# Optimization experiments

Measured on AMD Instinct MI355X. Metric: run time of the kernel, lower is better.

## Reference

```python
import jax, jax.numpy as jnp
import numpy as np

N_NODES = 50000


def _gcn_layer(x, src, dst, norm_src, norm_dst, W, b, act):
    # DGL GraphConv with norm='both': D_out^{-1/2} A D_in^{-1/2} X W + b
    h = x * norm_src[:, None]                      # scale by src out-degree
    m = h[src]                                     # gather messages [E, d]
    agg = jax.ops.segment_sum(m, dst, num_segments=N_NODES)  # scatter-add
    agg = agg * norm_dst[:, None]
    out = agg @ W + b
    if act:
        out = jax.nn.relu(out)
    return out


def setup_inputs() -> dict:
    key = jax.random.key(0)
    ks = jax.random.split(key, 10)
    E = 800000
    in_size, hid, out_size = 128, 128, 64
    features = jax.random.normal(ks[0], (N_NODES, in_size), dtype=jnp.float32)
    src = jax.random.randint(ks[1], (E,), 0, N_NODES, dtype=jnp.int32)
    dst = jax.random.randint(ks[2], (E,), 0, N_NODES, dtype=jnp.int32)
    s = 0.05
    W1 = jax.random.normal(ks[3], (in_size, hid), dtype=jnp.float32) * s
    b1 = jnp.zeros((hid,), dtype=jnp.float32)
    W2 = jax.random.normal(ks[4], (hid, hid), dtype=jnp.float32) * s
    b2 = jnp.zeros((hid,), dtype=jnp.float32)
    W3 = jax.random.normal(ks[5], (hid, out_size), dtype=jnp.float32) * s
    b3 = jnp.zeros((out_size,), dtype=jnp.float32)
    return {"features": features, "W1": W1, "b1": b1, "W2": W2, "b2": b2,
            "W3": W3, "b3": b3, "src": src, "dst": dst}


def reference(features, W1, b1, W2, b2, W3, b3, src, dst):
    ones = jnp.ones(src.shape, dtype=features.dtype)
    out_deg = jax.ops.segment_sum(ones, src, num_segments=N_NODES)
    in_deg = jax.ops.segment_sum(ones, dst, num_segments=N_NODES)
    norm_src = jnp.maximum(out_deg, 1.0) ** -0.5   # clamp(min=1) as in DGL
    norm_dst = jnp.maximum(in_deg, 1.0) ** -0.5
    h = _gcn_layer(features, src, dst, norm_src, norm_dst, W1, b1, act=True)
    # dropout is identity in eval mode
    h = _gcn_layer(h, src, dst, norm_src, norm_dst, W2, b2, act=True)
    h = _gcn_layer(h, src, dst, norm_src, norm_dst, W3, b3, act=False)
    return h
```

## Files before the change

kernel.cpp:

```cpp
#include <hip/hip_runtime.h>
#include <math.h>

#define N_NODES 50000
#define K_DIM 128
#define CAP 64
#define CHUNK 25000
#define RH 25000
#define HWORDS 12500

typedef __attribute__((ext_vector_type(8))) short short8_t;
typedef __attribute__((ext_vector_type(4))) float f32x4_t;
typedef __attribute__((ext_vector_type(8))) _Float16 half8_t;

__device__ inline unsigned short f2bf(float x) {
    unsigned u = __float_as_uint(x);
    unsigned r = u + 0x7fffu + ((u >> 16) & 1u);
    return (unsigned short)(r >> 16);
}
__device__ inline float bf2f(unsigned short h) {
    return __uint_as_float(((unsigned)h) << 16);
}

__global__ void init_zero_kernel(_Float16* Yx, _Float16* Yy, _Float16* Yz) {
    int t = threadIdx.x;
    if (t < 128) {
        Yx[(size_t)N_NODES * 128 + t] = (_Float16)0.f;
        Yy[(size_t)N_NODES * 128 + t] = (_Float16)0.f;
    }
    if (t < 64) Yz[(size_t)N_NODES * 64 + t] = (_Float16)0.f;
}


__global__ __launch_bounds__(1024) void hist_kernel(const int* __restrict__ src,
                                                    const int* __restrict__ dst, int E,
                                                    unsigned* __restrict__ pin,
                                                    unsigned* __restrict__ pout) {
    __shared__ unsigned h[HWORDS];
    int b  = blockIdx.x >> 2;
    int io = (blockIdx.x >> 1) & 1;
    int r  = blockIdx.x & 1;
    int tid = threadIdx.x;
    for (int t = tid; t < HWORDS; t += 1024) h[t] = 0;
    __syncthreads();
    const int* keys = io ? src : dst;
    int start = b * CHUNK;
    int end = start + CHUNK; if (end > E) end = E;
    int vlo = r * RH;
    for (int i = start + tid; i < end; i += 1024) {
        int v = keys[i] - vlo;
        if ((unsigned)v < (unsigned)RH)
            atomicAdd(&h[v >> 1], 1u << ((v & 1) * 16));
    }
    __syncthreads();
    unsigned* out = io ? pout : pin;
    for (int t = tid; t < HWORDS; t += 1024)
        out[(size_t)b * (2 * HWORDS) + r * HWORDS + t] = h[t];
}

__global__ void offsets_norm_kernel(const unsigned* __restrict__ pin,
                                    const unsigned* __restrict__ pout,
                                    unsigned short* __restrict__ off16,
                                    int* __restrict__ indeg,
                                    float* __restrict__ nsrc, float* __restrict__ ndst,
                                    int n, int NB) {
    int v = blockIdx.x * blockDim.x + threadIdx.x;
    if (v >= n) return;
    int wi = v >> 1, sh = (v & 1) * 16;
    int od = 0;
    for (int b = 0; b < NB; ++b)
        od += (pout[(size_t)b * (2 * HWORDS) + wi] >> sh) & 0xffff;
    int run = 0;
    for (int b = 0; b < NB; ++b) {
        int c = (pin[(size_t)b * (2 * HWORDS) + wi] >> sh) & 0xffff;
        off16[(size_t)b * n + v] = (unsigned short)(run < CAP ? run : CAP);
        run += c;
    }
    indeg[v] = run < CAP ? run : CAP;
    int odc = od < 1 ? 1 : od;
    int idc = run < 1 ? 1 : run;
    nsrc[v] = 1.0f / sqrtf((float)odc);
    ndst[v] = 1.0f / sqrtf((float)idc);
}

__global__ __launch_bounds__(1024) void scatter_kernel(const int* __restrict__ src,
                                                       const int* __restrict__ dst, int E,
                                                       const unsigned short* __restrict__ off16,
                                                       int* __restrict__ csr, int n) {
    __shared__ unsigned cur[HWORDS];
    int b = blockIdx.x >> 1;
    int r = blockIdx.x & 1;
    int tid = threadIdx.x;
    int vlo = r * RH;
    const unsigned short* offb = off16 + (size_t)b * n + vlo;
    for (int t = tid; t < HWORDS; t += 1024)
        cur[t] = (unsigned)offb[2 * t] | ((unsigned)offb[2 * t + 1] << 16);
    __syncthreads();
    int start = b * CHUNK;
    int end = start + CHUNK; if (end > E) end = E;
    for (int i = start + tid; i < end; i += 1024) {
        int v = dst[i];
        int vr = v - vlo;
        if ((unsigned)vr < (unsigned)RH) {
            int sh = (vr & 1) * 16;
            unsigned old = atomicAdd(&cur[vr >> 1], 1u << sh);
            unsigned p = (old >> sh) & 0xffff;
            if (p < CAP) csr[((size_t)v << 6) + p] = src[i];
        }
    }
}

__global__ void split_w_all_kernel(const float* __restrict__ W1,
                                   const float* __restrict__ W2,
                                   const float* __restrict__ W3,
                                   unsigned short* __restrict__ W1h, unsigned short* __restrict__ W1l,
                                   unsigned short* __restrict__ W2h, unsigned short* __restrict__ W2l,
                                   unsigned short* __restrict__ W3h, unsigned short* __restrict__ W3l) {
    int gi = blockIdx.x * blockDim.x + threadIdx.x;
    const float* W; unsigned short *WBh, *WBl; int M, i;
    if (gi < 2048)      { W = W1; WBh = W1h; WBl = W1l; M = 128; i = gi; }
    else if (gi < 4096) { W = W2; WBh = W2h; WBl = W2l; M = 128; i = gi - 2048; }
    else if (gi < 5120) { W = W3; WBh = W3h; WBl = W3l; M = 64;  i = gi - 4096; }
    else return;
    int c    = i >> 8;
    int rem  = i & 255;
    int kc   = rem >> 6;
    int lane = rem & 63;
    int m = lane & 15, q = lane >> 4;
    int n = c * 16 + m;
    #pragma unroll
    for (int j = 0; j < 8; ++j) {
        int k = kc * 32 + q * 8 + j;
        float w = W[(size_t)k * M + n];
        unsigned short hi = f2bf(w);
        unsigned short lo = f2bf(w - bf2f(hi));
        WBh[(size_t)i * 8 + j] = hi;
        WBl[(size_t)i * 8 + j] = lo;
    }
}

template <int M>
__global__ __launch_bounds__(256) void gemm_mfma_kernel(
        const float* __restrict__ X,
        const unsigned short* __restrict__ WBh_,
        const unsigned short* __restrict__ WBl_,
        const float* __restrict__ nsrc, _Float16* __restrict__ Yh, int n) {
    constexpr int LSTR = 136;
    __shared__ short Xhi[64 * LSTR];
    __shared__ short Xlo[64 * LSTR];
    int tid = threadIdx.x;
    int lane = tid & 63, wave = tid >> 6;
    int rowBlock = blockIdx.x * 64;

    #pragma unroll
    for (int l = 0; l < 8; ++l) {
        int idx = (tid + l * 256) * 4;
        int r = idx >> 7;
        int c = idx & 127;
        float4 v = make_float4(0.f, 0.f, 0.f, 0.f);
        int gr = rowBlock + r;
        if (gr < n) v = *(const float4*)&X[(size_t)gr * K_DIM + c];
        unsigned short h0 = f2bf(v.x), h1 = f2bf(v.y), h2 = f2bf(v.z), h3 = f2bf(v.w);
        short4 hs = {(short)h0, (short)h1, (short)h2, (short)h3};
        short4 ls = {(short)f2bf(v.x - bf2f(h0)), (short)f2bf(v.y - bf2f(h1)),
                     (short)f2bf(v.z - bf2f(h2)), (short)f2bf(v.w - bf2f(h3))};
        *(short4*)&Xhi[r * LSTR + c] = hs;
        *(short4*)&Xlo[r * LSTR + c] = ls;
    }
    __syncthreads();

    int m = lane & 15, q = lane >> 4;
    short8_t ah[4], al[4];
    {
        int abase = (wave * 16 + m) * LSTR + q * 8;
        #pragma unroll
        for (int kc = 0; kc < 4; ++kc) {
            ah[kc] = *(const short8_t*)&Xhi[abase + kc * 32];
            al[kc] = *(const short8_t*)&Xlo[abase + kc * 32];
        }
    }
    float ns[4];
    int orow0 = rowBlock + wave * 16 + q * 4;
    #pragma unroll
    for (int r = 0; r < 4; ++r) ns[r] = (orow0 + r < n) ? nsrc[orow0 + r] : 0.f;

    const short8_t* WBh = (const short8_t*)WBh_;
    const short8_t* WBl = (const short8_t*)WBl_;
    constexpr int CT = M / 16;
    #pragma unroll
    for (int c = 0; c < CT; ++c) {
        short8_t bh[4], bl[4];
        #pragma unroll
        for (int kc = 0; kc < 4; ++kc) {
            bh[kc] = WBh[(c * 4 + kc) * 64 + lane];
            bl[kc] = WBl[(c * 4 + kc) * 64 + lane];
        }
        f32x4_t acc = {0.f, 0.f, 0.f, 0.f};
        #pragma unroll
        for (int kc = 0; kc < 4; ++kc) {
            acc = __builtin_amdgcn_mfma_f32_16x16x32_bf16(ah[kc], bh[kc], acc, 0, 0, 0);
            acc = __builtin_amdgcn_mfma_f32_16x16x32_bf16(ah[kc], bl[kc], acc, 0, 0, 0);
            acc = __builtin_amdgcn_mfma_f32_16x16x32_bf16(al[kc], bh[kc], acc, 0, 0, 0);
        }
        int col = c * 16 + m;
        #pragma unroll
        for (int r = 0; r < 4; ++r) {
            int row = orow0 + r;
            if (row < n) Yh[(size_t)row * M + col] = (_Float16)(acc[r] * ns[r]);
        }
    }
}

template <int MOUT>
__global__ __launch_bounds__(256, 3) void agg_gemm_kernel(
        const _Float16* __restrict__ Yin,
        const int* __restrict__ indeg, const int* __restrict__ csr,
        const float* __restrict__ ndst, const float* __restrict__ bias,
        const unsigned short* __restrict__ WBh_,
        const unsigned short* __restrict__ WBl_,
        const float* __restrict__ nsrc, _Float16* __restrict__ Yout, int n) {
    constexpr int LSTR = 136;
    __shared__ short Xhi[32 * LSTR];
    __shared__ short Xlo[32 * LSTR];
    int tid = threadIdx.x;
    int lane = tid & 63, wave = tid >> 6;
    int rowBlock = blockIdx.x * 32;

    int sub = tid >> 4;
    int f8  = (tid & 15) * 8;
    #pragma unroll 1
    for (int p = 0; p < 2; ++p) {
        int r = p * 16 + sub;
        int v = rowBlock + r;
        float o[8] = {};
        if (v < n) {
            int deg = indeg[v];
            const int* __restrict__ row = &csr[(size_t)v * CAP];
            float acc[8] = {};
            #pragma unroll 1
            for (int i = 0; i < deg; i += 16) {
                int idx[16];
                #pragma unroll
                for (int t = 0; t < 16; t += 4) {
                    int4 s4 = *(const int4*)&row[i + t];
                    idx[t + 0] = s4.x; idx[t + 1] = s4.y;
                    idx[t + 2] = s4.z; idx[t + 3] = s4.w;
                }
                #pragma unroll
                for (int t = 1; t < 16; ++t)
                    if (i + t >= deg) idx[t] = N_NODES;
                half8_t g[16];
                #pragma unroll
                for (int t = 0; t < 16; ++t)
                    g[t] = *(const half8_t*)&Yin[(size_t)idx[t] * 128 + f8];
                #pragma unroll
                for (int t = 0; t < 16; ++t) {
                    #pragma unroll
                    for (int j = 0; j < 8; ++j) acc[j] += (float)g[t][j];
                }
            }
            float nd = ndst[v];
            #pragma unroll
            for (int j = 0; j < 8; ++j)
                o[j] = fmaxf(nd * acc[j] + bias[f8 + j], 0.f);
        }
        short hs[8], ls[8];
        #pragma unroll
        for (int j = 0; j < 8; ++j) {
            unsigned short h = f2bf(o[j]);
            hs[j] = (short)h;
            ls[j] = (short)f2bf(o[j] - bf2f(h));
        }
        *(short4*)&Xhi[r * LSTR + f8]     = *(short4*)&hs[0];
        *(short4*)&Xhi[r * LSTR + f8 + 4] = *(short4*)&hs[4];
        *(short4*)&Xlo[r * LSTR + f8]     = *(short4*)&ls[0];
        *(short4*)&Xlo[r * LSTR + f8 + 4] = *(short4*)&ls[4];
    }
    __syncthreads();

    int m = lane & 15, q = lane >> 4;
    int wrow = wave & 1;
    int wcol = wave >> 1;
    short8_t ah[4], al[4];
    {
        int abase = (wrow * 16 + m) * LSTR + q * 8;
        #pragma unroll
        for (int kc = 0; kc < 4; ++kc) {
            ah[kc] = *(const short8_t*)&Xhi[abase + kc * 32];
            al[kc] = *(const short8_t*)&Xlo[abase + kc * 32];
        }
    }
    float ns[4];
    int orow0 = rowBlock + wrow * 16 + q * 4;
    #pragma unroll
    for (int r = 0; r < 4; ++r) ns[r] = (orow0 + r < n) ? nsrc[orow0 + r] : 0.f;

    const short8_t* WBh = (const short8_t*)WBh_;
    const short8_t* WBl = (const short8_t*)WBl_;
    constexpr int CTH = MOUT / 32;
    #pragma unroll
    for (int c2 = 0; c2 < CTH; ++c2) {
        int c = wcol * CTH + c2;
        short8_t bh[4], bl[4];
        #pragma unroll
        for (int kc = 0; kc < 4; ++kc) {
            bh[kc] = WBh[(c * 4 + kc) * 64 + lane];
            bl[kc] = WBl[(c * 4 + kc) * 64 + lane];
        }
        f32x4_t acc = {0.f, 0.f, 0.f, 0.f};
        #pragma unroll
        for (int kc = 0; kc < 4; ++kc) {
            acc = __builtin_amdgcn_mfma_f32_16x16x32_bf16(ah[kc], bh[kc], acc, 0, 0, 0);
            acc = __builtin_amdgcn_mfma_f32_16x16x32_bf16(ah[kc], bl[kc], acc, 0, 0, 0);
            acc = __builtin_amdgcn_mfma_f32_16x16x32_bf16(al[kc], bh[kc], acc, 0, 0, 0);
        }
        int col = c * 16 + m;
        #pragma unroll
        for (int r = 0; r < 4; ++r) {
            int row = orow0 + r;
            if (row < n) Yout[(size_t)row * MOUT + col] = (_Float16)(acc[r] * ns[r]);
        }
    }
}

template <int M, bool RELU>
__global__ __launch_bounds__(256, 3) void agg_kernel(const _Float16* __restrict__ Y,
                                                     const int* __restrict__ indeg,
                                                     const int* __restrict__ csr,
                                                     const float* __restrict__ ndst,
                                                     const float* __restrict__ bias,
                                                     float* __restrict__ Z, int n) {
    constexpr int LPN = M / 8;
    constexpr int NPB = 256 / LPN;
    int v = blockIdx.x * NPB + threadIdx.x / LPN;
    if (v >= n) return;
    int f8 = (threadIdx.x % LPN) * 8;
    int deg = indeg[v];
    const int* __restrict__ row = &csr[(size_t)v * CAP];
    float acc[8] = {};
    #pragma unroll 1
    for (int i = 0; i < deg; i += 16) {
        int idx[16];
        #pragma unroll
        for (int t = 0; t < 16; t += 4) {
            int4 s4 = *(const int4*)&row[i + t];
            idx[t + 0] = s4.x; idx[t + 1] = s4.y;
            idx[t + 2] = s4.z; idx[t + 3] = s4.w;
        }
        #pragma unroll
        for (int t = 1; t < 16; ++t)
            if (i + t >= deg) idx[t] = N_NODES;
        half8_t g[16];
        #pragma unroll
        for (int t = 0; t < 16; ++t)
            g[t] = *(const half8_t*)&Y[(size_t)idx[t] * M + f8];
        #pragma unroll
        for (int t = 0; t < 16; ++t) {
            #pragma unroll
            for (int j = 0; j < 8; ++j) acc[j] += (float)g[t][j];
        }
    }
    float nd = ndst[v];
    float4 bb0 = *(const float4*)&bias[f8];
    float4 bb1 = *(const float4*)&bias[f8 + 4];
    float o[8];
    o[0] = nd * acc[0] + bb0.x; o[1] = nd * acc[1] + bb0.y;
    o[2] = nd * acc[2] + bb0.z; o[3] = nd * acc[3] + bb0.w;
    o[4] = nd * acc[4] + bb1.x; o[5] = nd * acc[5] + bb1.y;
    o[6] = nd * acc[6] + bb1.z; o[7] = nd * acc[7] + bb1.w;
    if (RELU) {
        #pragma unroll
        for (int j = 0; j < 8; ++j) o[j] = fmaxf(o[j], 0.f);
    }
    *(float4*)&Z[(size_t)v * M + f8]     = make_float4(o[0], o[1], o[2], o[3]);
    *(float4*)&Z[(size_t)v * M + f8 + 4] = make_float4(o[4], o[5], o[6], o[7]);
}


extern "C" void kernel_launch(void* const* d_in, const int* in_sizes, int n_in,
                              void* d_out, int out_size, void* d_ws, size_t ws_size,
                              hipStream_t stream) {
    const float* features = (const float*)d_in[0];
    const float* W1 = (const float*)d_in[1];
    const float* b1 = (const float*)d_in[2];
    const float* W2 = (const float*)d_in[3];
    const float* b2 = (const float*)d_in[4];
    const float* W3 = (const float*)d_in[5];
    const float* b3 = (const float*)d_in[6];
    const int* src = (const int*)d_in[7];
    const int* dst = (const int*)d_in[8];
    const int E = in_sizes[7];
    const int N = N_NODES;
    const int NB = (E + CHUNK - 1) / CHUNK;

    char* w = (char*)d_ws;
    auto alloc = [&](size_t bytes) {
        char* p = w;
        w += (bytes + 255) & ~(size_t)255;
        return p;
    };
    _Float16* Yx = (_Float16*)alloc((size_t)(N + 1) * 128 * 2);
    _Float16* Yy = (_Float16*)alloc((size_t)(N + 1) * 128 * 2);
    _Float16* Yz = (_Float16*)alloc((size_t)(N + 1) * 64 * 2);
    int*   csr    = (int*)alloc((size_t)N * CAP * 4);
    unsigned* pin  = (unsigned*)alloc((size_t)NB * 2 * HWORDS * 4);
    unsigned* pout = (unsigned*)alloc((size_t)NB * 2 * HWORDS * 4);
    unsigned short* off16 = (unsigned short*)alloc((size_t)NB * N * 2);
    int*   indeg  = (int*)alloc((size_t)N * 4);
    float* nsrc   = (float*)alloc((size_t)N * 4);
    float* ndst   = (float*)alloc((size_t)N * 4);
    unsigned short* W1h = (unsigned short*)alloc(128 * 128 * 2);
    unsigned short* W1l = (unsigned short*)alloc(128 * 128 * 2);
    unsigned short* W2h = (unsigned short*)alloc(128 * 128 * 2);
    unsigned short* W2l = (unsigned short*)alloc(128 * 128 * 2);
    unsigned short* W3h = (unsigned short*)alloc(64 * 128 * 2);
    unsigned short* W3l = (unsigned short*)alloc(64 * 128 * 2);

    init_zero_kernel<<<1, 128, 0, stream>>>(Yx, Yy, Yz);
    hist_kernel<<<NB * 4, 1024, 0, stream>>>(src, dst, E, pin, pout);
    offsets_norm_kernel<<<(N + 255) / 256, 256, 0, stream>>>(pin, pout, off16, indeg,
                                                             nsrc, ndst, N, NB);
    scatter_kernel<<<NB * 2, 1024, 0, stream>>>(src, dst, E, off16, csr, N);
    split_w_all_kernel<<<20, 256, 0, stream>>>(W1, W2, W3, W1h, W1l, W2h, W2l, W3h, W3l);

    int gblocks64 = (N + 63) / 64;
    int gblocks32 = (N + 31) / 32;
    gemm_mfma_kernel<128><<<gblocks64, 256, 0, stream>>>(features, W1h, W1l, nsrc, Yx, N);
    agg_gemm_kernel<128><<<gblocks32, 256, 0, stream>>>(Yx, indeg, csr, ndst, b1,
                                                        W2h, W2l, nsrc, Yy, N);
    agg_gemm_kernel<64><<<gblocks32, 256, 0, stream>>>(Yy, indeg, csr, ndst, b2,
                                                       W3h, W3l, nsrc, Yz, N);
    agg_kernel<64, false><<<(N + 31) / 32, 256, 0, stream>>>(Yz, indeg, csr, ndst, b3,
                                                             (float*)d_out, N);
}
```

Measured before the change: 239.8 us.

## Replace LDS histogram CSR build with direct global-atomic scatter

The multi-pass CSR construction is replaced by one pass of global atomics. The old pass did per-chunk LDS histograms, a prefix over chunks and then an LDS-cursor scatter. Now a single kernel counts out-degree and claims in-edge slots with atomicAdd on per-node counters. Zeroing is merged into one prep kernel, and normalisation and weight splitting into one finalize kernel, cutting the launch count and the intermediate partial-histogram buffers. The trade-off is global atomic contention, and neighbour order within each CSR row is no longer deterministic, so summation order can vary.

Result: slower. 258.4 us (+7.8%).

```diff
diff --git a/kernel.cpp b/kernel.cpp
--- a/kernel.cpp
+++ b/kernel.cpp
@@ -4,9 +4,6 @@
 #define N_NODES 50000
 #define K_DIM 128
 #define CAP 64
-#define CHUNK 25000
-#define RH 25000
-#define HWORDS 12500
 
 typedef __attribute__((ext_vector_type(8))) short short8_t;
 typedef __attribute__((ext_vector_type(4))) float f32x4_t;
@@ -21,101 +18,55 @@
     return __uint_as_float(((unsigned)h) << 16);
 }
 
-__global__ void init_zero_kernel(_Float16* Yx, _Float16* Yy, _Float16* Yz) {
-    int t = threadIdx.x;
-    if (t < 128) {
-        Yx[(size_t)N_NODES * 128 + t] = (_Float16)0.f;
-        Yy[(size_t)N_NODES * 128 + t] = (_Float16)0.f;
-    }
-    if (t < 64) Yz[(size_t)N_NODES * 64 + t] = (_Float16)0.f;
-}
-
-
-__global__ __launch_bounds__(1024) void hist_kernel(const int* __restrict__ src,
-                                                    const int* __restrict__ dst, int E,
-                                                    unsigned* __restrict__ pin,
-                                                    unsigned* __restrict__ pout) {
-    __shared__ unsigned h[HWORDS];
-    int b  = blockIdx.x >> 2;
-    int io = (blockIdx.x >> 1) & 1;
-    int r  = blockIdx.x & 1;
-    int tid = threadIdx.x;
-    for (int t = tid; t < HWORDS; t += 1024) h[t] = 0;
-    __syncthreads();
-    const int* keys = io ? src : dst;
-    int start = b * CHUNK;
-    int end = start + CHUNK; if (end > E) end = E;
-    int vlo = r * RH;
-    for (int i = start + tid; i < end; i += 1024) {
-        int v = keys[i] - vlo;
-        if ((unsigned)v < (unsigned)RH)
-            atomicAdd(&h[v >> 1], 1u << ((v & 1) * 16));
-    }
-    __syncthreads();
-    unsigned* out = io ? pout : pin;
-    for (int t = tid; t < HWORDS; t += 1024)
-        out[(size_t)b * (2 * HWORDS) + r * HWORDS + t] = h[t];
-}
-
-__global__ void offsets_norm_kernel(const unsigned* __restrict__ pin,
-                                    const unsigned* __restrict__ pout,
-                                    unsigned short* __restrict__ off16,
-                                    int* __restrict__ indeg,
-                                    float* __restrict__ nsrc, float* __restrict__ ndst,
-                                    int n, int NB) {
-    int v = blockIdx.x * blockDim.x + threadIdx.x;
-    if (v >= n) return;
-    int wi = v >> 1, sh = (v & 1) * 16;
-    int od = 0;
-    for (int b = 0; b < NB; ++b)
-        od += (pout[(size_t)b * (2 * HWORDS) + wi] >> sh) & 0xffff;
-    int run = 0;
-    for (int b = 0; b < NB; ++b) {
-        int c = (pin[(size_t)b * (2 * HWORDS) + wi] >> sh) & 0xffff;
-        off16[(size_t)b * n + v] = (unsigned short)(run < CAP ? run : CAP);
-        run += c;
-    }
-    indeg[v] = run < CAP ? run : CAP;
-    int odc = od < 1 ? 1 : od;
-    int idc = run < 1 ? 1 : run;
-    nsrc[v] = 1.0f / sqrtf((float)odc);
-    ndst[v] = 1.0f / sqrtf((float)idc);
-}
-
-__global__ __launch_bounds__(1024) void scatter_kernel(const int* __restrict__ src,
-                                                       const int* __restrict__ dst, int E,
-                                                       const unsigned short* __restrict__ off16,
-                                                       int* __restrict__ csr, int n) {
-    __shared__ unsigned cur[HWORDS];
-    int b = blockIdx.x >> 1;
-    int r = blockIdx.x & 1;
-    int tid = threadIdx.x;
-    int vlo = r * RH;
-    const unsigned short* offb = off16 + (size_t)b * n + vlo;
-    for (int t = tid; t < HWORDS; t += 1024)
-        cur[t] = (unsigned)offb[2 * t] | ((unsigned)offb[2 * t + 1] << 16);
-    __syncthreads();
-    int start = b * CHUNK;
-    int end = start + CHUNK; if (end > E) end = E;
-    for (int i = start + tid; i < end; i += 1024) {
-        int v = dst[i];
-        int vr = v - vlo;
-        if ((unsigned)vr < (unsigned)RH) {
-            int sh = (vr & 1) * 16;
-            unsigned old = atomicAdd(&cur[vr >> 1], 1u << sh);
-            unsigned p = (old >> sh) & 0xffff;
-            if (p < CAP) csr[((size_t)v << 6) + p] = src[i];
-        }
-    }
-}
-
-__global__ void split_w_all_kernel(const float* __restrict__ W1,
-                                   const float* __restrict__ W2,
-                                   const float* __restrict__ W3,
-                                   unsigned short* __restrict__ W1h, unsigned short* __restrict__ W1l,
-                                   unsigned short* __restrict__ W2h, unsigned short* __restrict__ W2l,
-                                   unsigned short* __restrict__ W3h, unsigned short* __restrict__ W3l) {
-    int gi = blockIdx.x * blockDim.x + threadIdx.x;
+__global__ __launch_bounds__(256) void prep_kernel(unsigned* __restrict__ cur,
+                                                   unsigned* __restrict__ cnt_out,
+                                                   _Float16* Yx, _Float16* Yy, _Float16* Yz) {
+    int i = blockIdx.x * 256 + threadIdx.x;
+    if (i < N_NODES) { cur[i] = 0u; cnt_out[i] = 0u; }
+    if (blockIdx.x == 0) {
+        int t = threadIdx.x;
+        if (t < 128) {
+            Yx[(size_t)N_NODES * 128 + t] = (_Float16)0.f;
+            Yy[(size_t)N_NODES * 128 + t] = (_Float16)0.f;
+        }
+        if (t < 64) Yz[(size_t)N_NODES * 64 + t] = (_Float16)0.f;
+    }
+}
+
+__global__ __launch_bounds__(256) void scatter_count_kernel(const int* __restrict__ src,
+                                                            const int* __restrict__ dst, int E,
+                                                            unsigned* __restrict__ cnt_out,
+                                                            unsigned* __restrict__ cur,
+                                                            int* __restrict__ csr) {
+    int i = blockIdx.x * 256 + threadIdx.x;
+    if (i >= E) return;
+    int s = src[i], d = dst[i];
+    atomicAdd(&cnt_out[s], 1u);
+    unsigned p = atomicAdd(&cur[d], 1u);
+    if (p < CAP) csr[((size_t)d << 6) + p] = s;
+}
+
+__global__ __launch_bounds__(256) void finalize_kernel(
+        const unsigned* __restrict__ cur, const unsigned* __restrict__ cnt_out,
+        int* __restrict__ indeg, float* __restrict__ nsrc, float* __restrict__ ndst,
+        const float* __restrict__ W1, const float* __restrict__ W2,
+        const float* __restrict__ W3,
+        unsigned short* __restrict__ W1h, unsigned short* __restrict__ W1l,
+        unsigned short* __restrict__ W2h, unsigned short* __restrict__ W2l,
+        unsigned short* __restrict__ W3h, unsigned short* __restrict__ W3l) {
+    if (blockIdx.x < 196) {
+        int v = blockIdx.x * 256 + threadIdx.x;
+        if (v >= N_NODES) return;
+        unsigned id = cur[v];
+        unsigned od = cnt_out[v];
+        indeg[v] = (int)(id < CAP ? id : CAP);
+        unsigned odc = od < 1u ? 1u : od;
+        unsigned idc = id < 1u ? 1u : id;
+        nsrc[v] = 1.0f / sqrtf((float)odc);
+        ndst[v] = 1.0f / sqrtf((float)idc);
+        return;
+    }
+    int gi = (blockIdx.x - 196) * 256 + threadIdx.x;
     const float* W; unsigned short *WBh, *WBl; int M, i;
     if (gi < 2048)      { W = W1; WBh = W1h; WBl = W1l; M = 128; i = gi; }
     else if (gi < 4096) { W = W2; WBh = W2h; WBl = W2l; M = 128; i = gi - 2048; }
@@ -390,7 +341,6 @@
     const int* dst = (const int*)d_in[8];
     const int E = in_sizes[7];
     const int N = N_NODES;
-    const int NB = (E + CHUNK - 1) / CHUNK;
 
     char* w = (char*)d_ws;
     auto alloc = [&](size_t bytes) {
@@ -402,9 +352,8 @@
     _Float16* Yy = (_Float16*)alloc((size_t)(N + 1) * 128 * 2);
     _Float16* Yz = (_Float16*)alloc((size_t)(N + 1) * 64 * 2);
     int*   csr    = (int*)alloc((size_t)N * CAP * 4);
-    unsigned* pin  = (unsigned*)alloc((size_t)NB * 2 * HWORDS * 4);
-    unsigned* pout = (unsigned*)alloc((size_t)NB * 2 * HWORDS * 4);
-    unsigned short* off16 = (unsigned short*)alloc((size_t)NB * N * 2);
+    unsigned* cnt_out = (unsigned*)alloc((size_t)N * 4);
+    unsigned* cur     = (unsigned*)alloc((size_t)N * 4);
     int*   indeg  = (int*)alloc((size_t)N * 4);
     float* nsrc   = (float*)alloc((size_t)N * 4);
     float* ndst   = (float*)alloc((size_t)N * 4);
@@ -415,12 +364,11 @@
     unsigned short* W3h = (unsigned short*)alloc(64 * 128 * 2);
     unsigned short* W3l = (unsigned short*)alloc(64 * 128 * 2);
 
-    init_zero_kernel<<<1, 128, 0, stream>>>(Yx, Yy, Yz);
-    hist_kernel<<<NB * 4, 1024, 0, stream>>>(src, dst, E, pin, pout);
-    offsets_norm_kernel<<<(N + 255) / 256, 256, 0, stream>>>(pin, pout, off16, indeg,
-                                                             nsrc, ndst, N, NB);
-    scatter_kernel<<<NB * 2, 1024, 0, stream>>>(src, dst, E, off16, csr, N);
-    split_w_all_kernel<<<20, 256, 0, stream>>>(W1, W2, W3, W1h, W1l, W2h, W2l, W3h, W3l);
+    prep_kernel<<<196, 256, 0, stream>>>(cur, cnt_out, Yx, Yy, Yz);
+    scatter_count_kernel<<<(E + 255) / 256, 256, 0, stream>>>(src, dst, E,
+                                                              cnt_out, cur, csr);
+    finalize_kernel<<<216, 256, 0, stream>>>(cur, cnt_out, indeg, nsrc, ndst,
+                                             W1, W2, W3, W1h, W1l, W2h, W2l, W3h, W3l);
 
     int gblocks64 = (N + 63) / 64;
     int gblocks32 = (N + 31) / 32;
```

## Merge setup kernels, co-schedule scatter with first GEMM, shrink CSR to uint16

Applied to the files above, without the earlier changes.

Folds the zero-init and weight-split work into the histogram kernel. The CSR scatter and the first-layer GEMM now run in one launch, with separate block ranges and a shared LDS buffer, so the two can overlap. CSR neighbor indices are stored as 16-bit values, halving the index traffic in the three aggregation kernels. Launch count drops by three. The GEMM path uses 512-thread blocks holding two 64-row sub-tiles, which needs more LDS per block. The 16-bit indices only work while node IDs fit in 65535, which holds for 50000 nodes.

Result: faster. 228.3 us (-4.8%).

```diff
diff --git a/kernel.cpp b/kernel.cpp
--- a/kernel.cpp
+++ b/kernel.cpp
@@ -9,6 +9,7 @@
 #define HWORDS 12500
 
 typedef __attribute__((ext_vector_type(8))) short short8_t;
+typedef __attribute__((ext_vector_type(8))) unsigned short ushort8_t;
 typedef __attribute__((ext_vector_type(4))) float f32x4_t;
 typedef __attribute__((ext_vector_type(8))) _Float16 half8_t;
 
@@ -21,40 +22,68 @@
     return __uint_as_float(((unsigned)h) << 16);
 }
 
-__global__ void init_zero_kernel(_Float16* Yx, _Float16* Yy, _Float16* Yz) {
-    int t = threadIdx.x;
-    if (t < 128) {
-        Yx[(size_t)N_NODES * 128 + t] = (_Float16)0.f;
-        Yy[(size_t)N_NODES * 128 + t] = (_Float16)0.f;
-    }
-    if (t < 64) Yz[(size_t)N_NODES * 64 + t] = (_Float16)0.f;
-}
-
-
-__global__ __launch_bounds__(1024) void hist_kernel(const int* __restrict__ src,
-                                                    const int* __restrict__ dst, int E,
-                                                    unsigned* __restrict__ pin,
-                                                    unsigned* __restrict__ pout) {
-    __shared__ unsigned h[HWORDS];
-    int b  = blockIdx.x >> 2;
-    int io = (blockIdx.x >> 1) & 1;
-    int r  = blockIdx.x & 1;
+__global__ __launch_bounds__(1024) void hist_init_split_kernel(
+        const int* __restrict__ src, const int* __restrict__ dst, int E,
+        unsigned* __restrict__ pin, unsigned* __restrict__ pout,
+        _Float16* Yx, _Float16* Yy, _Float16* Yz,
+        const float* __restrict__ W1, const float* __restrict__ W2,
+        const float* __restrict__ W3,
+        unsigned short* __restrict__ W1h, unsigned short* __restrict__ W1l,
+        unsigned short* __restrict__ W2h, unsigned short* __restrict__ W2l,
+        unsigned short* __restrict__ W3h, unsigned short* __restrict__ W3l,
+        int NBLK) {
     int tid = threadIdx.x;
-    for (int t = tid; t < HWORDS; t += 1024) h[t] = 0;
-    __syncthreads();
-    const int* keys = io ? src : dst;
-    int start = b * CHUNK;
-    int end = start + CHUNK; if (end > E) end = E;
-    int vlo = r * RH;
-    for (int i = start + tid; i < end; i += 1024) {
-        int v = keys[i] - vlo;
-        if ((unsigned)v < (unsigned)RH)
-            atomicAdd(&h[v >> 1], 1u << ((v & 1) * 16));
-    }
-    __syncthreads();
-    unsigned* out = io ? pout : pin;
-    for (int t = tid; t < HWORDS; t += 1024)
-        out[(size_t)b * (2 * HWORDS) + r * HWORDS + t] = h[t];
+    if (blockIdx.x < (unsigned)(NBLK * 4)) {
+        __shared__ unsigned h[HWORDS];
+        int b  = blockIdx.x >> 2;
+        int io = (blockIdx.x >> 1) & 1;
+        int r  = blockIdx.x & 1;
+        for (int t = tid; t < HWORDS; t += 1024) h[t] = 0;
+        __syncthreads();
+        const int* keys = io ? src : dst;
+        int start = b * CHUNK;
+        int end = start + CHUNK; if (end > E) end = E;
+        int vlo = r * RH;
+        for (int i = start + tid; i < end; i += 1024) {
+            int v = keys[i] - vlo;
+            if ((unsigned)v < (unsigned)RH)
+                atomicAdd(&h[v >> 1], 1u << ((v & 1) * 16));
+        }
+        __syncthreads();
+        unsigned* out = io ? pout : pin;
+        for (int t = tid; t < HWORDS; t += 1024)
+            out[(size_t)b * (2 * HWORDS) + r * HWORDS + t] = h[t];
+        return;
+    }
+    if (blockIdx.x == (unsigned)(NBLK * 4)) {
+        if (tid < 128) {
+            Yx[(size_t)N_NODES * 128 + tid] = (_Float16)0.f;
+            Yy[(size_t)N_NODES * 128 + tid] = (_Float16)0.f;
+        }
+        if (tid < 64) Yz[(size_t)N_NODES * 64 + tid] = (_Float16)0.f;
+        return;
+    }
+    int gi = (blockIdx.x - (NBLK * 4 + 1)) * 1024 + tid;
+    const float* W; unsigned short *WBh, *WBl; int M, i;
+    if (gi < 2048)      { W = W1; WBh = W1h; WBl = W1l; M = 128; i = gi; }
+    else if (gi < 4096) { W = W2; WBh = W2h; WBl = W2l; M = 128; i = gi - 2048; }
+    else if (gi < 5120) { W = W3; WBh = W3h; WBl = W3l; M = 64;  i = gi - 4096; }
+    else return;
+    int c    = i >> 8;
+    int rem  = i & 255;
+    int kc   = rem >> 6;
+    int lane = rem & 63;
+    int m = lane & 15, q = lane >> 4;
+    int n = c * 16 + m;
+    #pragma unroll
+    for (int j = 0; j < 8; ++j) {
+        int k = kc * 32 + q * 8 + j;
+        float w = W[(size_t)k * M + n];
+        unsigned short hi = f2bf(w);
+        unsigned short lo = f2bf(w - bf2f(hi));
+        WBh[(size_t)i * 8 + j] = hi;
+        WBl[(size_t)i * 8 + j] = lo;
+    }
 }
 
 __global__ void offsets_norm_kernel(const unsigned* __restrict__ pin,
@@ -82,78 +111,53 @@
     ndst[v] = 1.0f / sqrtf((float)idc);
 }
 
-__global__ __launch_bounds__(1024) void scatter_kernel(const int* __restrict__ src,
-                                                       const int* __restrict__ dst, int E,
-                                                       const unsigned short* __restrict__ off16,
-                                                       int* __restrict__ csr, int n) {
-    __shared__ unsigned cur[HWORDS];
-    int b = blockIdx.x >> 1;
-    int r = blockIdx.x & 1;
-    int tid = threadIdx.x;
-    int vlo = r * RH;
-    const unsigned short* offb = off16 + (size_t)b * n + vlo;
-    for (int t = tid; t < HWORDS; t += 1024)
-        cur[t] = (unsigned)offb[2 * t] | ((unsigned)offb[2 * t + 1] << 16);
-    __syncthreads();
-    int start = b * CHUNK;
-    int end = start + CHUNK; if (end > E) end = E;
-    for (int i = start + tid; i < end; i += 1024) {
-        int v = dst[i];
-        int vr = v - vlo;
-        if ((unsigned)vr < (unsigned)RH) {
-            int sh = (vr & 1) * 16;
-            unsigned old = atomicAdd(&cur[vr >> 1], 1u << sh);
-            unsigned p = (old >> sh) & 0xffff;
-            if (p < CAP) csr[((size_t)v << 6) + p] = src[i];
-        }
-    }
-}
-
-__global__ void split_w_all_kernel(const float* __restrict__ W1,
-                                   const float* __restrict__ W2,
-                                   const float* __restrict__ W3,
-                                   unsigned short* __restrict__ W1h, unsigned short* __restrict__ W1l,
-                                   unsigned short* __restrict__ W2h, unsigned short* __restrict__ W2l,
-                                   unsigned short* __restrict__ W3h, unsigned short* __restrict__ W3l) {
-    int gi = blockIdx.x * blockDim.x + threadIdx.x;
-    const float* W; unsigned short *WBh, *WBl; int M, i;
-    if (gi < 2048)      { W = W1; WBh = W1h; WBl = W1l; M = 128; i = gi; }
-    else if (gi < 4096) { W = W2; WBh = W2h; WBl = W2l; M = 128; i = gi - 2048; }
-    else if (gi < 5120) { W = W3; WBh = W3h; WBl = W3l; M = 64;  i = gi - 4096; }
-    else return;
-    int c    = i >> 8;
-    int rem  = i & 255;
-    int kc   = rem >> 6;
-    int lane = rem & 63;
-    int m = lane & 15, q = lane >> 4;
-    int n = c * 16 + m;
-    #pragma unroll
-    for (int j = 0; j < 8; ++j) {
-        int k = kc * 32 + q * 8 + j;
-        float w = W[(size_t)k * M + n];
-        unsigned short hi = f2bf(w);
-        unsigned short lo = f2bf(w - bf2f(hi));
-        WBh[(size_t)i * 8 + j] = hi;
-        WBl[(size_t)i * 8 + j] = lo;
-    }
-}
-
-template <int M>
-__global__ __launch_bounds__(256) void gemm_mfma_kernel(
+__global__ __launch_bounds__(512) void scatter_gemm_kernel(
+        const int* __restrict__ src, const int* __restrict__ dst, int E,
+        const unsigned short* __restrict__ off16,
+        unsigned short* __restrict__ csr, int n, int NB2,
         const float* __restrict__ X,
         const unsigned short* __restrict__ WBh_,
         const unsigned short* __restrict__ WBl_,
-        const float* __restrict__ nsrc, _Float16* __restrict__ Yh, int n) {
+        const float* __restrict__ nsrc, _Float16* __restrict__ Yh) {
+    __shared__ unsigned smemu[17408];
+    int tid = threadIdx.x;
+
+    if (blockIdx.x < (unsigned)NB2) {
+        unsigned* cur = smemu;
+        int b = blockIdx.x >> 1;
+        int r = blockIdx.x & 1;
+        int vlo = r * RH;
+        const unsigned short* offb = off16 + (size_t)b * n + vlo;
+        for (int t = tid; t < HWORDS; t += 512)
+            cur[t] = (unsigned)offb[2 * t] | ((unsigned)offb[2 * t + 1] << 16);
+        __syncthreads();
+        int start = b * CHUNK;
+        int end = start + CHUNK; if (end > E) end = E;
+        for (int i = start + tid; i < end; i += 512) {
+            int v = dst[i];
+            int vr = v - vlo;
+            if ((unsigned)vr < (unsigned)RH) {
+                int sh = (vr & 1) * 16;
+                unsigned old = atomicAdd(&cur[vr >> 1], 1u << sh);
+                unsigned p = (old >> sh) & 0xffff;
+                if (p < CAP) csr[((size_t)v << 6) + p] = (unsigned short)src[i];
+            }
+        }
+        return;
+    }
+
     constexpr int LSTR = 136;
-    __shared__ short Xhi[64 * LSTR];
-    __shared__ short Xlo[64 * LSTR];
-    int tid = threadIdx.x;
-    int lane = tid & 63, wave = tid >> 6;
-    int rowBlock = blockIdx.x * 64;
+    int s    = tid >> 8;
+    int stid = tid & 255;
+    short* Xhi = (short*)smemu + s * 17408;
+    short* Xlo = Xhi + 64 * LSTR;
+    int gb = blockIdx.x - NB2;
+    int rowBlock = gb * 128 + s * 64;
+    int lane = stid & 63, wave = stid >> 6;
 
     #pragma unroll
     for (int l = 0; l < 8; ++l) {
-        int idx = (tid + l * 256) * 4;
+        int idx = (stid + l * 256) * 4;
         int r = idx >> 7;
         int c = idx & 127;
         float4 v = make_float4(0.f, 0.f, 0.f, 0.f);
@@ -185,9 +189,8 @@
 
     const short8_t* WBh = (const short8_t*)WBh_;
     const short8_t* WBl = (const short8_t*)WBl_;
-    constexpr int CT = M / 16;
-    #pragma unroll
-    for (int c = 0; c < CT; ++c) {
+    #pragma unroll
+    for (int c = 0; c < 8; ++c) {
         short8_t bh[4], bl[4];
         #pragma unroll
         for (int kc = 0; kc < 4; ++kc) {
@@ -205,7 +208,7 @@
         #pragma unroll
         for (int r = 0; r < 4; ++r) {
             int row = orow0 + r;
-            if (row < n) Yh[(size_t)row * M + col] = (_Float16)(acc[r] * ns[r]);
+            if (row < n) Yh[(size_t)row * 128 + col] = (_Float16)(acc[r] * ns[r]);
         }
     }
 }
@@ -213,7 +216,7 @@
 template <int MOUT>
 __global__ __launch_bounds__(256, 3) void agg_gemm_kernel(
         const _Float16* __restrict__ Yin,
-        const int* __restrict__ indeg, const int* __restrict__ csr,
+        const int* __restrict__ indeg, const unsigned short* __restrict__ csr,
         const float* __restrict__ ndst, const float* __restrict__ bias,
         const unsigned short* __restrict__ WBh_,
         const unsigned short* __restrict__ WBl_,
@@ -234,17 +237,17 @@
         float o[8] = {};
         if (v < n) {
             int deg = indeg[v];
-            const int* __restrict__ row = &csr[(size_t)v * CAP];
+            const unsigned short* __restrict__ row = &csr[(size_t)v * CAP];
             float acc[8] = {};
             #pragma unroll 1
             for (int i = 0; i < deg; i += 16) {
+                ushort8_t ia = *(const ushort8_t*)&row[i];
+                ushort8_t ib = *(const ushort8_t*)&row[i + 8];
                 int idx[16];
                 #pragma unroll
-                for (int t = 0; t < 16; t += 4) {
-                    int4 s4 = *(const int4*)&row[i + t];
-                    idx[t + 0] = s4.x; idx[t + 1] = s4.y;
-                    idx[t + 2] = s4.z; idx[t + 3] = s4.w;
-                }
+                for (int t = 0; t < 8; ++t) idx[t] = (int)ia[t];
+                #pragma unroll
+                for (int t = 0; t < 8; ++t) idx[8 + t] = (int)ib[t];
                 #pragma unroll
                 for (int t = 1; t < 16; ++t)
                     if (i + t >= deg) idx[t] = N_NODES;
@@ -325,7 +328,7 @@
 template <int M, bool RELU>
 __global__ __launch_bounds__(256, 3) void agg_kernel(const _Float16* __restrict__ Y,
                                                      const int* __restrict__ indeg,
-                                                     const int* __restrict__ csr,
+                                                     const unsigned short* __restrict__ csr,
                                                      const float* __restrict__ ndst,
                                                      const float* __restrict__ bias,
                                                      float* __restrict__ Z, int n) {
@@ -335,17 +338,17 @@
     if (v >= n) return;
     int f8 = (threadIdx.x % LPN) * 8;
     int deg = indeg[v];
-    const int* __restrict__ row = &csr[(size_t)v * CAP];
+    const unsigned short* __restrict__ row = &csr[(size_t)v * CAP];
     float acc[8] = {};
     #pragma unroll 1
     for (int i = 0; i < deg; i += 16) {
+        ushort8_t ia = *(const ushort8_t*)&row[i];
+        ushort8_t ib = *(const ushort8_t*)&row[i + 8];
         int idx[16];
         #pragma unroll
-        for (int t = 0; t < 16; t += 4) {
-            int4 s4 = *(const int4*)&row[i + t];
-            idx[t + 0] = s4.x; idx[t + 1] = s4.y;
-            idx[t + 2] = s4.z; idx[t + 3] = s4.w;
-        }
+        for (int t = 0; t < 8; ++t) idx[t] = (int)ia[t];
+        #pragma unroll
+        for (int t = 0; t < 8; ++t) idx[8 + t] = (int)ib[t];
         #pragma unroll
         for (int t = 1; t < 16; ++t)
             if (i + t >= deg) idx[t] = N_NODES;
@@ -401,7 +404,7 @@
     _Float16* Yx = (_Float16*)alloc((size_t)(N + 1) * 128 * 2);
     _Float16* Yy = (_Float16*)alloc((size_t)(N + 1) * 128 * 2);
     _Float16* Yz = (_Float16*)alloc((size_t)(N + 1) * 64 * 2);
-    int*   csr    = (int*)alloc((size_t)N * CAP * 4);
+    unsigned short* csr = (unsigned short*)alloc((size_t)N * CAP * 2);
     unsigned* pin  = (unsigned*)alloc((size_t)NB * 2 * HWORDS * 4);
     unsigned* pout = (unsigned*)alloc((size_t)NB * 2 * HWORDS * 4);
     unsigned short* off16 = (unsigned short*)alloc((size_t)NB * N * 2);
@@ -415,20 +418,21 @@
     unsigned short* W3h = (unsigned short*)alloc(64 * 128 * 2);
     unsigned short* W3l = (unsigned short*)alloc(64 * 128 * 2);
 
-    init_zero_kernel<<<1, 128, 0, stream>>>(Yx, Yy, Yz);
-    hist_kernel<<<NB * 4, 1024, 0, stream>>>(src, dst, E, pin, pout);
+    hist_init_split_kernel<<<NB * 4 + 1 + 5, 1024, 0, stream>>>(
+        src, dst, E, pin, pout, Yx, Yy, Yz,
+        W1, W2, W3, W1h, W1l, W2h, W2l, W3h, W3l, NB);
     offsets_norm_kernel<<<(N + 255) / 256, 256, 0, stream>>>(pin, pout, off16, indeg,
                                                              nsrc, ndst, N, NB);
-    scatter_kernel<<<NB * 2, 1024, 0, stream>>>(src, dst, E, off16, csr, N);
-    split_w_all_kernel<<<20, 256, 0, stream>>>(W1, W2, W3, W1h, W1l, W2h, W2l, W3h, W3l);
-
-    int gblocks64 = (N + 63) / 64;
+    int gemmBlocks = (N + 127) / 128;
+    scatter_gemm_kernel<<<NB * 2 + gemmBlocks, 512, 0, stream>>>(
+        src, dst, E, off16, csr, N, NB * 2,
+        features, W1h, W1l, nsrc, Yx);
+
     int gblocks32 = (N + 31) / 32;
-    gemm_mfma_kernel<128><<<gblocks64, 256, 0, stream>>>(features, W1h, W1l, nsrc, Yx, N);
     agg_gemm_kernel<128><<<gblocks32, 256, 0, stream>>>(Yx, indeg, csr, ndst, b1,
                                                         W2h, W2l, nsrc, Yy, N);
     agg_gemm_kernel<64><<<gblocks32, 256, 0, stream>>>(Yy, indeg, csr, ndst, b2,
                                                        W3h, W3l, nsrc, Yz, N);
-    agg_kernel<64, false><<<(N + 31) / 32, 256, 0, stream>>>(Yz, indeg, csr, ndst, b3,
-                                                             (float*)d_out, N);
-}
+    agg_kernel<64, false><<<gblocks32, 256, 0, stream>>>(Yz, indeg, csr, ndst, b3,
+                                                         (float*)d_out, N);
+}
```
